# Optimization experiments

Measured on AMD Instinct MI355X. Metric: run time of the kernel, lower is better.

The kernel has to match this reference:

```python
import jax, jax.numpy as jnp
import numpy as np

B, S, DIM, H = 2, 2048, 2048, 16
HD = DIM // H  # head_dim = 128
EPS = 1e-6


def setup_inputs() -> dict:
    key = jax.random.key(0)
    ks = jax.random.split(key, 13)
    d = {
        'hidden_states': jax.random.normal(ks[0], (B, S, DIM), jnp.float32),
        'freqs_cos': jax.random.normal(ks[1], (1, S, 1, HD), jnp.float32),
        'freqs_sin': jax.random.normal(ks[2], (1, S, 1, HD), jnp.float32),
        'Wq': jax.random.normal(ks[3], (DIM, DIM), jnp.float32) * 0.02,
        'bq': jax.random.normal(ks[4], (DIM,), jnp.float32) * 0.02,
        'Wk': jax.random.normal(ks[5], (DIM, DIM), jnp.float32) * 0.02,
        'bk': jax.random.normal(ks[6], (DIM,), jnp.float32) * 0.02,
        'Wv': jax.random.normal(ks[7], (DIM, DIM), jnp.float32) * 0.02,
        'bv': jax.random.normal(ks[8], (DIM,), jnp.float32) * 0.02,
        'norm_q_w': jax.random.uniform(ks[9], (DIM,), jnp.float32, 0.5, 1.5),
        'norm_k_w': jax.random.uniform(ks[10], (DIM,), jnp.float32, 0.5, 1.5),
        'Wo': jax.random.normal(ks[11], (DIM, DIM), jnp.float32) * 0.02,
        'bo': jax.random.normal(ks[12], (DIM,), jnp.float32) * 0.02,
    }
    return d


def _rms_norm(x, w, eps=EPS):
    # local RMSNorm over the full inner_dim (no cross-rank reduce)
    xf = x.astype(jnp.float32)
    var = jnp.mean(xf * xf, axis=-1, keepdims=True)
    return (w * (xf * jax.lax.rsqrt(var + eps))).astype(x.dtype)


def _apply_rope(x, freqs_cos, freqs_sin):
    # x: [B,H,S,D]; freqs: [1,S,1,D] -> broadcast cos/sin at [1,1,S,D/2]
    dtype = x.dtype
    xf = x.astype(jnp.float32)
    x1 = xf[..., 0::2]
    x2 = xf[..., 1::2]
    cos = jnp.transpose(freqs_cos[..., 0::2], (0, 2, 1, 3)).astype(jnp.float32)
    sin = jnp.transpose(freqs_sin[..., 1::2], (0, 2, 1, 3)).astype(jnp.float32)
    even = x1 * cos - x2 * sin
    odd = x1 * sin + x2 * cos
    out = jnp.stack([even, odd], axis=-1).reshape(x.shape)
    return out.astype(dtype)


def reference(hidden_states, freqs_cos, freqs_sin, Wq, bq, Wk, bk, Wv, bv,
              norm_q_w, norm_k_w, Wo, bo):
    b, s, _ = hidden_states.shape
    q = hidden_states @ Wq.T + bq
    k = hidden_states @ Wk.T + bk
    v = hidden_states @ Wv.T + bv
    q = _rms_norm(q, norm_q_w)
    k = _rms_norm(k, norm_k_w)
    # [B,S,H*D] -> [B,H,S,D]
    q = q.reshape(b, s, H, HD).transpose(0, 2, 1, 3)
    k = k.reshape(b, s, H, HD).transpose(0, 2, 1, 3)
    v = v.reshape(b, s, H, HD).transpose(0, 2, 1, 3)
    q = _apply_rope(q, freqs_cos, freqs_sin)
    k = _apply_rope(k, freqs_cos, freqs_sin)
    # flash attention math (full, non-causal), scale = 1/sqrt(head_dim)
    scale = 1.0 / np.sqrt(HD).astype(np.float32)
    scores = jnp.einsum('bhqd,bhkd->bhqk', q, k) * scale
    attn = jax.nn.softmax(scores, axis=-1)
    out = jnp.einsum('bhqk,bhkd->bhqd', attn, v)
    out = out.transpose(0, 2, 1, 3).reshape(b, s, H * HD)
    return out @ Wo.T + bo
```

## Files before the change

### kernel.cpp

```cpp
#include <hip/hip_runtime.h>
#include <stdint.h>

#define DEVI __device__ __forceinline__

typedef __attribute__((ext_vector_type(8))) short bf16x8;
typedef __attribute__((ext_vector_type(4))) float f32x4;
typedef __attribute__((ext_vector_type(16))) float f32x16;
typedef __attribute__((ext_vector_type(4))) unsigned short u16x4;
typedef __attribute__((ext_vector_type(8))) unsigned short u16x8;

DEVI unsigned short f2bf(float f) {
    union { float f; unsigned u; } v; v.f = f;
    unsigned r = v.u + 0x7fffu + ((v.u >> 16) & 1u);
    return (unsigned short)(r >> 16);
}

DEVI float bf2f(unsigned short u) {
    union { unsigned u; float f; } v; v.u = ((unsigned)u) << 16;
    return v.f;
}

DEVI unsigned cvtpk(float lo, float hi) {
    unsigned r;
    asm("v_cvt_pk_bf16_f32 %0, %1, %2" : "=v"(r) : "v"(lo), "v"(hi));
    return r;
}

DEVI void gload16(const void* g, void* lds) {
    __builtin_amdgcn_global_load_lds(
        (const __attribute__((address_space(1))) unsigned int*)(uintptr_t)g,
        (__attribute__((address_space(3))) unsigned int*)(unsigned int)(uintptr_t)lds,
        16, 0, 0);
}

__global__ __launch_bounds__(256) void cvt_all(
    const float* __restrict__ hs, const float* __restrict__ wq,
    const float* __restrict__ wk, const float* __restrict__ wv,
    const float* __restrict__ wo,
    unsigned short* __restrict__ o_hs, unsigned short* __restrict__ o_wq,
    unsigned short* __restrict__ o_wk, unsigned short* __restrict__ o_wv,
    unsigned short* __restrict__ o_wo) {
    const int bid = blockIdx.x;
    const float* src; unsigned short* dst; int base;
    if (bid < 2048)      { src = hs; dst = o_hs; base = bid; }
    else if (bid < 3072) { src = wq; dst = o_wq; base = bid - 2048; }
    else if (bid < 4096) { src = wk; dst = o_wk; base = bid - 3072; }
    else if (bid < 5120) { src = wv; dst = o_wv; base = bid - 4096; }
    else                 { src = wo; dst = o_wo; base = bid - 5120; }
    const int i0 = base * 1024 + threadIdx.x;
#pragma unroll
    for (int k = 0; k < 4; k++) {
        const int i = i0 + k * 256;
        float4 v = ((const float4*)src)[i];
        u16x4 pk;
        pk[0] = f2bf(v.x); pk[1] = f2bf(v.y); pk[2] = f2bf(v.z); pk[3] = f2bf(v.w);
        ((u16x4*)dst)[i] = pk;
    }
}

DEVI void gemm_pipe_core(const unsigned short* __restrict__ A,
                         const unsigned short* __restrict__ Wt,
                         int m0, int n0, char* lds,
                         f32x4 (&acc)[2][2][2][2]) {
    constexpr int K = 2048;
    const int t = threadIdx.x;
    const int w = t >> 6, l = t & 63, lr = l & 15, lk = l >> 4;
    const int wr = w >> 2, wc = w & 3;
    const int sx = lr & 7;
    const int srow = t >> 3, sseg = (t & 7) ^ (srow & 7);
    const unsigned short* aS = A + (size_t)(m0 + srow) * K + sseg * 8;
    const unsigned short* bS = Wt + (size_t)(n0 + srow) * K + sseg * 8;
    char* Bbase = lds + 32768;

#pragma unroll
    for (int qm = 0; qm < 2; qm++)
#pragma unroll
        for (int qn = 0; qn < 2; qn++)
#pragma unroll
            for (int fr = 0; fr < 2; fr++)
#pragma unroll
                for (int fc = 0; fc < 2; fc++)
                    acc[qm][qn][fr][fc] = (f32x4){0.f, 0.f, 0.f, 0.f};

    auto STAGE = [&](int tt, int u) {
        if (tt >= 32) return;
        const int k0 = tt * 64, bb = tt & 1;
        if (u < 4)
            gload16(bS + (size_t)u * 64 * K + k0, Bbase + bb * 32768 + u * 8192 + w * 1024);
        else
            gload16(aS + (size_t)(u - 4) * 64 * K + k0, lds + bb * 16384 + (u - 4) * 8192 + w * 1024);
    };

    STAGE(0, 0); STAGE(0, 1); STAGE(0, 2); STAGE(0, 3); STAGE(0, 4); STAGE(0, 5);
    STAGE(1, 0); STAGE(1, 1); STAGE(1, 2);
    asm volatile("s_waitcnt vmcnt(3)" ::: "memory");
    __builtin_amdgcn_s_barrier();

    for (int kt = 0; kt < 32; ++kt) {
        const int bb = kt & 1;
        const char* Ab = lds + bb * 16384;
        const char* Bb = Bbase + bb * 32768;
        bf16x8 a0[2][2], a1[2][2], b0[2][2], b1[2][2];
#pragma unroll
        for (int fr = 0; fr < 2; fr++)
#pragma unroll
            for (int ks = 0; ks < 2; ks++) {
                a0[fr][ks] = *(const bf16x8*)(Ab + (wr * 64 + fr * 16 + lr) * 128 +
                                              (((ks * 4 + lk) ^ sx) << 4));
                a1[fr][ks] = *(const bf16x8*)(Ab + (wr * 64 + 32 + fr * 16 + lr) * 128 +
                                              (((ks * 4 + lk) ^ sx) << 4));
            }
#pragma unroll
        for (int fc = 0; fc < 2; fc++)
#pragma unroll
            for (int ks = 0; ks < 2; ks++) {
                b0[fc][ks] = *(const bf16x8*)(Bb + (wc * 64 + fc * 16 + lr) * 128 +
                                              (((ks * 4 + lk) ^ sx) << 4));
                b1[fc][ks] = *(const bf16x8*)(Bb + (wc * 64 + 32 + fc * 16 + lr) * 128 +
                                              (((ks * 4 + lk) ^ sx) << 4));
            }
        STAGE(kt + 1, 3); STAGE(kt + 1, 4); STAGE(kt + 1, 5);
        __builtin_amdgcn_s_setprio(1);
#pragma unroll
        for (int ks = 0; ks < 2; ks++)
#pragma unroll
            for (int fr = 0; fr < 2; fr++)
#pragma unroll
                for (int fc = 0; fc < 2; fc++) {
                    acc[0][0][fr][fc] = __builtin_amdgcn_mfma_f32_16x16x32_bf16(
                        a0[fr][ks], b0[fc][ks], acc[0][0][fr][fc], 0, 0, 0);
                    acc[1][0][fr][fc] = __builtin_amdgcn_mfma_f32_16x16x32_bf16(
                        a1[fr][ks], b0[fc][ks], acc[1][0][fr][fc], 0, 0, 0);
                }
        __builtin_amdgcn_s_setprio(0);
        asm volatile("s_waitcnt lgkmcnt(0)" ::: "memory");
        __builtin_amdgcn_s_barrier();
        STAGE(kt + 2, 0); STAGE(kt + 2, 1); STAGE(kt + 2, 2);
        __builtin_amdgcn_s_setprio(1);
#pragma unroll
        for (int ks = 0; ks < 2; ks++)
#pragma unroll
            for (int fr = 0; fr < 2; fr++)
#pragma unroll
                for (int fc = 0; fc < 2; fc++) {
                    acc[0][1][fr][fc] = __builtin_amdgcn_mfma_f32_16x16x32_bf16(
                        a0[fr][ks], b1[fc][ks], acc[0][1][fr][fc], 0, 0, 0);
                    acc[1][1][fr][fc] = __builtin_amdgcn_mfma_f32_16x16x32_bf16(
                        a1[fr][ks], b1[fc][ks], acc[1][1][fr][fc], 0, 0, 0);
                }
        __builtin_amdgcn_s_setprio(0);
        if (kt < 30)       asm volatile("s_waitcnt vmcnt(3)" ::: "memory");
        else if (kt == 30) asm volatile("s_waitcnt vmcnt(0)" ::: "memory");
        __builtin_amdgcn_s_barrier();
    }
}

__global__ __launch_bounds__(512, 2) void gemm_qkv(
    const unsigned short* __restrict__ A,
    const unsigned short* __restrict__ Wq16, const unsigned short* __restrict__ Wk16,
    const unsigned short* __restrict__ Wv16,
    const float* __restrict__ bq, const float* __restrict__ bk, const float* __restrict__ bv,
    unsigned short* __restrict__ qh, unsigned short* __restrict__ kh,
    unsigned short* __restrict__ Vt) {
    __shared__ char Lds[98304];
    const int bid = blockIdx.x;
    const int nt = bid & 7, rem = bid >> 3;
    const int mt = rem / 3, z = rem % 3;
    const int m0 = mt * 128, n0 = nt * 256;
    const unsigned short* W = (z == 0) ? Wq16 : (z == 1) ? Wk16 : Wv16;
    const float* bias = (z == 0) ? bq : (z == 1) ? bk : bv;

    f32x4 acc[2][2][2][2];
    gemm_pipe_core(A, W, m0, n0, Lds, acc);

    const int t = threadIdx.x, w = t >> 6, l = t & 63, lr = l & 15, lk = l >> 4;
    const int wr = w >> 2, wc = w & 3;
#pragma unroll
    for (int qm = 0; qm < 2; qm++)
#pragma unroll
        for (int qn = 0; qn < 2; qn++)
#pragma unroll
            for (int fr = 0; fr < 2; fr++)
#pragma unroll
                for (int fc = 0; fc < 2; fc++) {
                    const int col = n0 + wc * 64 + qn * 32 + fc * 16 + lr;
                    const int rb = m0 + wr * 64 + qm * 32 + fr * 16 + lk * 4;
                    const float bb = bias[col];
                    if (z == 2) {
                        const int hh = col >> 7, d = col & 127;
                        const int b = rb >> 11, s = rb & 2047;
                        u16x4 pk;
#pragma unroll
                        for (int j = 0; j < 4; j++) pk[j] = f2bf(acc[qm][qn][fr][fc][j] + bb);
                        *(u16x4*)(Vt + ((size_t)((b * 16 + hh) * 128 + d)) * 2048 + s) = pk;
                    } else {
                        unsigned short* out = (z == 0) ? qh : kh;
#pragma unroll
                        for (int j = 0; j < 4; j++)
                            out[(size_t)(rb + j) * 2048 + col] = f2bf(acc[qm][qn][fr][fc][j] + bb);
                    }
                }
}

__global__ __launch_bounds__(512, 2) void gemm_o(
    const unsigned short* __restrict__ A, const unsigned short* __restrict__ W16,
    const float* __restrict__ bo, float* __restrict__ out) {
    __shared__ char Lds[98304];
    const int bid = blockIdx.x;
    const int nt = bid & 7, mt = bid >> 3;
    const int m0 = mt * 128, n0 = nt * 256;

    f32x4 acc[2][2][2][2];
    gemm_pipe_core(A, W16, m0, n0, Lds, acc);

    const int t = threadIdx.x, w = t >> 6, l = t & 63, lr = l & 15, lk = l >> 4;
    const int wr = w >> 2, wc = w & 3;
#pragma unroll
    for (int qm = 0; qm < 2; qm++)
#pragma unroll
        for (int qn = 0; qn < 2; qn++)
#pragma unroll
            for (int fr = 0; fr < 2; fr++)
#pragma unroll
                for (int fc = 0; fc < 2; fc++) {
                    const int col = n0 + wc * 64 + qn * 32 + fc * 16 + lr;
                    const int rb = m0 + wr * 64 + qm * 32 + fr * 16 + lk * 4;
                    const float bb = bo[col];
#pragma unroll
                    for (int j = 0; j < 4; j++)
                        out[(size_t)(rb + j) * 2048 + col] = acc[qm][qn][fr][fc][j] + bb;
                }
}

__global__ __launch_bounds__(256) void norm_rope(
    const unsigned short* __restrict__ qh, const unsigned short* __restrict__ kh,
    const float* __restrict__ nqw, const float* __restrict__ nkw,
    const float* __restrict__ fc, const float* __restrict__ fs,
    unsigned short* __restrict__ Qr, unsigned short* __restrict__ Kr) {
    const int row = blockIdx.x;
    const int which = blockIdx.y;
    const unsigned short* in = which ? kh : qh;
    const float* wv = which ? nkw : nqw;
    unsigned short* out = which ? Kr : Qr;
    const float qs = which ? 1.0f : 0.12751744f;
    const int t = threadIdx.x;
    u16x8 xr = *(const u16x8*)(in + (size_t)row * 2048 + t * 8);
    float xv[8];
#pragma unroll
    for (int e = 0; e < 8; e++) xv[e] = bf2f(xr[e]);
    float ss = 0.f;
#pragma unroll
    for (int e = 0; e < 8; e++) ss += xv[e] * xv[e];
#pragma unroll
    for (int m = 1; m < 64; m <<= 1) ss += __shfl_xor(ss, m, 64);
    __shared__ float red[4];
    if ((t & 63) == 0) red[t >> 6] = ss;
    __syncthreads();
    const float tot = red[0] + red[1] + red[2] + red[3];
    const float r = rsqrtf(tot * (1.0f / 2048.0f) + 1e-6f);
    const int s = row & 2047, b = row >> 11;
    const int d0 = t * 8, hd0 = d0 & 127, h = d0 >> 7;
    float4 c0 = ((const float4*)(fc + s * 128 + hd0))[0];
    float4 c1 = ((const float4*)(fc + s * 128 + hd0))[1];
    float4 s0 = ((const float4*)(fs + s * 128 + hd0))[0];
    float4 s1 = ((const float4*)(fs + s * 128 + hd0))[1];
    float4 w0 = ((const float4*)(wv + d0))[0];
    float4 w1 = ((const float4*)(wv + d0))[1];
    float wn[8] = {w0.x, w0.y, w0.z, w0.w, w1.x, w1.y, w1.z, w1.w};
    float xn[8];
#pragma unroll
    for (int e = 0; e < 8; e++) xn[e] = xv[e] * wn[e] * r;
    float o[8];
    o[0] = xn[0] * c0.x - xn[1] * s0.y;  o[1] = xn[0] * s0.y + xn[1] * c0.x;
    o[2] = xn[2] * c0.z - xn[3] * s0.w;  o[3] = xn[2] * s0.w + xn[3] * c0.z;
    o[4] = xn[4] * c1.x - xn[5] * s1.y;  o[5] = xn[4] * s1.y + xn[5] * c1.x;
    o[6] = xn[6] * c1.z - xn[7] * s1.w;  o[7] = xn[6] * s1.w + xn[7] * c1.z;
    u16x8 pk;
#pragma unroll
    for (int e = 0; e < 8; e++) pk[e] = f2bf(o[e] * qs);
    *(u16x8*)(out + ((size_t)((b * 16 + h) * 2048 + s)) * 128 + hd0) = pk;
}

__global__ __launch_bounds__(256, 2) void attn(
    const unsigned short* __restrict__ Qr, const unsigned short* __restrict__ Kr,
    const unsigned short* __restrict__ Vt, unsigned short* __restrict__ Ao) {
    __shared__ unsigned short Kl[2][64 * 128];
    __shared__ unsigned short Vl[2][128 * 64];
    const int t = threadIdx.x, w = t >> 6, l = t & 63;
    const int ql = l & 31, h = l >> 5;
    const int bid = blockIdx.x;
    const int xcd = bid & 7, idx = bid >> 3;
    const int bh = xcd * 4 + (idx >> 4);
    const int q0 = (idx & 15) * 128 + w * 32;
    const int b = bh >> 4, head = bh & 15;

    const unsigned short* Qp = Qr + ((size_t)bh * 2048 + q0) * 128;
    bf16x8 qf[8];
#pragma unroll
    for (int c8 = 0; c8 < 8; c8++)
        qf[c8] = *(const bf16x8*)(Qp + ql * 128 + c8 * 16 + h * 8);

    f32x16 accO[4];
#pragma unroll
    for (int dt = 0; dt < 4; dt++)
#pragma unroll
        for (int r = 0; r < 16; r++) accO[dt][r] = 0.f;
    float mj = -1e30f, ljp = 0.f;

    const unsigned short* Kb = Kr + (size_t)bh * 2048 * 128;
    const unsigned short* Vb = Vt + (size_t)bh * 128 * 2048;
    const int krow = t >> 4, kseg = (t & 15) ^ (krow & 7);
    const int vrow = t >> 3, vseg = (t & 7) ^ (vrow & 7);

    auto STAGE = [&](int buf, int kv0) {
        char* kd = (char*)&Kl[buf][0] + w * 1024;
        char* vd = (char*)&Vl[buf][0] + w * 1024;
#pragma unroll
        for (int c = 0; c < 4; c++)
            gload16(Kb + (size_t)(kv0 + c * 16 + krow) * 128 + kseg * 8, kd + c * 4096);
#pragma unroll
        for (int c = 0; c < 4; c++)
            gload16(Vb + (size_t)(c * 32 + vrow) * 2048 + kv0 + vseg * 8, vd + c * 4096);
    };

    const int qx = ql & 7;
    STAGE(0, 0);
    __syncthreads();
    int cur = 0;
    for (int it = 0; it < 32; ++it) {
        if (it < 31) STAGE(cur ^ 1, (it + 1) * 64);
        f32x16 S0, S1;
#pragma unroll
        for (int r = 0; r < 16; r++) { S0[r] = 0.f; S1[r] = 0.f; }
        __builtin_amdgcn_s_setprio(1);
#pragma unroll
        for (int c8 = 0; c8 < 8; c8++) {
            const int sg = ((c8 * 2 + h) ^ qx) << 4;
            bf16x8 k0 = *(const bf16x8*)((const char*)&Kl[cur][0] + ql * 256 + sg);
            bf16x8 k1 = *(const bf16x8*)((const char*)&Kl[cur][0] + (32 + ql) * 256 + sg);
            S0 = __builtin_amdgcn_mfma_f32_32x32x16_bf16(k0, qf[c8], S0, 0, 0, 0);
            S1 = __builtin_amdgcn_mfma_f32_32x32x16_bf16(k1, qf[c8], S1, 0, 0, 0);
        }
        __builtin_amdgcn_s_setprio(0);
        float mloc = S0[0];
#pragma unroll
        for (int r = 1; r < 16; r++) mloc = fmaxf(mloc, S0[r]);
#pragma unroll
        for (int r = 0; r < 16; r++) mloc = fmaxf(mloc, S1[r]);
        const float mx = fmaxf(mloc, __shfl_xor(mloc, 32, 64));
        if (!__all(mx <= mj + 8.0f)) {
            const float mn = fmaxf(mj, mx);
            const float corr = exp2f(mj - mn);
            mj = mn;
            ljp *= corr;
#pragma unroll
            for (int dt = 0; dt < 4; dt++)
#pragma unroll
                for (int r = 0; r < 16; r++) accO[dt][r] *= corr;
        }
        unsigned W[16];
        float lsum = 0.f;
#pragma unroll
        for (int i = 0; i < 8; i++) {
            const float pa = exp2f(S0[2 * i] - mj);
            const float pb = exp2f(S0[2 * i + 1] - mj);
            W[i] = cvtpk(pa, pb);
            lsum += pa + pb;
        }
#pragma unroll
        for (int i = 0; i < 8; i++) {
            const float pa = exp2f(S1[2 * i] - mj);
            const float pb = exp2f(S1[2 * i + 1] - mj);
            W[8 + i] = cvtpk(pa, pb);
            lsum += pa + pb;
        }
        ljp += lsum;
#pragma unroll
        for (int c = 0; c < 2; c++) {
            unsigned X[8];
#pragma unroll
            for (int i = 0; i < 8; i++)
                X[i] = (unsigned)__shfl_xor((int)W[c * 8 + i], 32, 64);
            union U { unsigned u[4]; bf16x8 v; };
            U F, G;
            F.u[0] = h ? X[2] : W[c * 8 + 0];
            F.u[1] = h ? X[3] : W[c * 8 + 1];
            F.u[2] = h ? W[c * 8 + 2] : X[0];
            F.u[3] = h ? W[c * 8 + 3] : X[1];
            G.u[0] = h ? X[6] : W[c * 8 + 4];
            G.u[1] = h ? X[7] : W[c * 8 + 5];
            G.u[2] = h ? W[c * 8 + 6] : X[4];
            G.u[3] = h ? W[c * 8 + 7] : X[5];
            __builtin_amdgcn_s_setprio(1);
#pragma unroll
            for (int dt = 0; dt < 4; dt++) {
                const int sg = (((2 * c) * 2 + h) ^ qx) << 4;
                bf16x8 vf = *(const bf16x8*)((const char*)&Vl[cur][0] + (dt * 32 + ql) * 128 + sg);
                accO[dt] = __builtin_amdgcn_mfma_f32_32x32x16_bf16(vf, F.v, accO[dt], 0, 0, 0);
            }
#pragma unroll
            for (int dt = 0; dt < 4; dt++) {
                const int sg = (((2 * c + 1) * 2 + h) ^ qx) << 4;
                bf16x8 vf = *(const bf16x8*)((const char*)&Vl[cur][0] + (dt * 32 + ql) * 128 + sg);
                accO[dt] = __builtin_amdgcn_mfma_f32_32x32x16_bf16(vf, G.v, accO[dt], 0, 0, 0);
            }
            __builtin_amdgcn_s_setprio(0);
        }
        __syncthreads();
        cur ^= 1;
    }
    const float lj = ljp + __shfl_xor(ljp, 32, 64);
    const float inv = 1.0f / lj;
    unsigned short* ob = Ao + ((size_t)(b * 2048 + q0 + ql)) * 2048 + head * 128;
#pragma unroll
    for (int dt = 0; dt < 4; dt++)
#pragma unroll
        for (int i = 0; i < 8; i++) {
            const float a = accO[dt][2 * i] * inv;
            const float c = accO[dt][2 * i + 1] * inv;
            const int d = dt * 32 + ((2 * i) & 3) + 8 * (i >> 1) + 4 * h;
            *(unsigned*)(ob + d) = cvtpk(a, c);
        }
}

extern "C" void kernel_launch(void* const* d_in, const int* in_sizes, int n_in,
                              void* d_out, int out_size, void* d_ws, size_t ws_size,
                              hipStream_t stream) {
    const float* hs  = (const float*)d_in[0];
    const float* fc  = (const float*)d_in[1];
    const float* fs  = (const float*)d_in[2];
    const float* Wq  = (const float*)d_in[3];
    const float* bq  = (const float*)d_in[4];
    const float* Wk  = (const float*)d_in[5];
    const float* bk  = (const float*)d_in[6];
    const float* Wv  = (const float*)d_in[7];
    const float* bv  = (const float*)d_in[8];
    const float* nqw = (const float*)d_in[9];
    const float* nkw = (const float*)d_in[10];
    const float* Wo  = (const float*)d_in[11];
    const float* bo  = (const float*)d_in[12];
    float* out = (float*)d_out;

    char* p = (char*)d_ws;
    unsigned short* hs16 = (unsigned short*)p; p += (size_t)8388608 * 2;
    unsigned short* Wq16 = (unsigned short*)p; p += (size_t)4194304 * 2;
    unsigned short* Wk16 = (unsigned short*)p; p += (size_t)4194304 * 2;
    unsigned short* Wv16 = (unsigned short*)p; p += (size_t)4194304 * 2;
    unsigned short* Wo16 = (unsigned short*)p; p += (size_t)4194304 * 2;
    unsigned short* qh = (unsigned short*)p;   p += (size_t)8388608 * 2;
    unsigned short* kh = (unsigned short*)p;   p += (size_t)8388608 * 2;
    unsigned short* Qr = (unsigned short*)p;   p += (size_t)8388608 * 2;
    unsigned short* Kr = (unsigned short*)p;   p += (size_t)8388608 * 2;
    unsigned short* Vt = (unsigned short*)p;   p += (size_t)8388608 * 2;
    unsigned short* Ao = (unsigned short*)p;   p += (size_t)8388608 * 2;
    (void)ws_size; (void)in_sizes; (void)n_in; (void)out_size;

    cvt_all<<<6144, 256, 0, stream>>>(hs, Wq, Wk, Wv, Wo,
                                      hs16, Wq16, Wk16, Wv16, Wo16);
    gemm_qkv<<<768, 512, 0, stream>>>(hs16, Wq16, Wk16, Wv16,
                                      bq, bk, bv, qh, kh, Vt);
    norm_rope<<<dim3(4096, 2), 256, 0, stream>>>(qh, kh, nqw, nkw, fc, fs, Qr, Kr);
    attn<<<512, 256, 0, stream>>>(Qr, Kr, Vt, Ao);
    gemm_o<<<256, 512, 0, stream>>>(Ao, Wo16, bo, out);
}
```

Before: 297.5 us.

## Use 256x256 output tiles with a new pipelined core for QKV GEMM

Adds a new GEMM core that computes 256x256 output tiles per block, each wave holding an 8x4 grid of 16x16 MFMA accumulators, with double-buffered LDS of 128KB. The QKV projection grid is halved to 384 blocks and the block index mapping changes so the M tile comes first. The aim is higher arithmetic intensity per LDS and global load, which cuts A/B reloads. In exchange it uses more registers and LDS per block, so occupancy drops, and 384 blocks may fill the 256 CUs unevenly.

```diff
diff --git a/kernel.cpp b/kernel.cpp
--- a/kernel.cpp
+++ b/kernel.cpp
@@ -58,6 +58,83 @@
     }
 }
 
+DEVI void gemm_core256(const unsigned short* __restrict__ A,
+                       const unsigned short* __restrict__ Wt,
+                       int m0, int n0, char* lds,
+                       f32x4 (&acc)[8][4]) {
+    constexpr int K = 2048;
+    const int t = threadIdx.x;
+    const int w = t >> 6, l = t & 63, lr = l & 15, lk = l >> 4;
+    const int wr = w >> 2, wc = w & 3;
+    const int sx = lr & 7;
+    const int srow = t >> 3, sseg = (t & 7) ^ (srow & 7);
+    const unsigned short* aS = A + (size_t)(m0 + srow) * K + sseg * 8;
+    const unsigned short* bS = Wt + (size_t)(n0 + srow) * K + sseg * 8;
+
+#pragma unroll
+    for (int mi = 0; mi < 8; mi++)
+#pragma unroll
+        for (int ni = 0; ni < 4; ni++) acc[mi][ni] = (f32x4){0.f, 0.f, 0.f, 0.f};
+
+    auto STAGE = [&](int tt, int u) {
+        if (tt >= 32) return;
+        const int k0 = tt * 64, bb = tt & 1;
+        if (u < 4)
+            gload16(aS + (size_t)u * 64 * K + k0, lds + bb * 32768 + u * 8192 + w * 1024);
+        else
+            gload16(bS + (size_t)(u - 4) * 64 * K + k0,
+                    lds + 65536 + bb * 32768 + (u - 4) * 8192 + w * 1024);
+    };
+
+    STAGE(0, 0); STAGE(0, 1); STAGE(0, 2); STAGE(0, 3);
+    STAGE(0, 4); STAGE(0, 5); STAGE(0, 6); STAGE(0, 7);
+    STAGE(1, 0); STAGE(1, 1); STAGE(1, 2); STAGE(1, 3);
+    asm volatile("s_waitcnt vmcnt(4)" ::: "memory");
+    __builtin_amdgcn_s_barrier();
+
+    for (int kt = 0; kt < 32; ++kt) {
+        const int bb = kt & 1;
+        const char* Ab = lds + bb * 32768;
+        const char* Bb = lds + 65536 + bb * 32768;
+        bf16x8 a[8][2], b[4][2];
+#pragma unroll
+        for (int mi = 0; mi < 8; mi++)
+#pragma unroll
+            for (int ks = 0; ks < 2; ks++)
+                a[mi][ks] = *(const bf16x8*)(Ab + (wr * 128 + mi * 16 + lr) * 128 +
+                                             (((ks * 4 + lk) ^ sx) << 4));
+#pragma unroll
+        for (int ni = 0; ni < 4; ni++)
+#pragma unroll
+            for (int ks = 0; ks < 2; ks++)
+                b[ni][ks] = *(const bf16x8*)(Bb + (wc * 64 + ni * 16 + lr) * 128 +
+                                             (((ks * 4 + lk) ^ sx) << 4));
+        STAGE(kt + 1, 4); STAGE(kt + 1, 5); STAGE(kt + 1, 6); STAGE(kt + 1, 7);
+        __builtin_amdgcn_s_setprio(1);
+#pragma unroll
+        for (int mi = 0; mi < 8; mi++)
+#pragma unroll
+            for (int ni = 0; ni < 4; ni++)
+                acc[mi][ni] = __builtin_amdgcn_mfma_f32_16x16x32_bf16(
+                    a[mi][0], b[ni][0], acc[mi][ni], 0, 0, 0);
+        __builtin_amdgcn_s_setprio(0);
+        asm volatile("s_waitcnt lgkmcnt(0)" ::: "memory");
+        __builtin_amdgcn_s_barrier();
+        STAGE(kt + 2, 0); STAGE(kt + 2, 1); STAGE(kt + 2, 2); STAGE(kt + 2, 3);
+        __builtin_amdgcn_s_setprio(1);
+#pragma unroll
+        for (int mi = 0; mi < 8; mi++)
+#pragma unroll
+            for (int ni = 0; ni < 4; ni++)
+                acc[mi][ni] = __builtin_amdgcn_mfma_f32_16x16x32_bf16(
+                    a[mi][1], b[ni][1], acc[mi][ni], 0, 0, 0);
+        __builtin_amdgcn_s_setprio(0);
+        if (kt < 30)       asm volatile("s_waitcnt vmcnt(4)" ::: "memory");
+        else if (kt == 30) asm volatile("s_waitcnt vmcnt(0)" ::: "memory");
+        __builtin_amdgcn_s_barrier();
+    }
+}
+
 DEVI void gemm_pipe_core(const unsigned short* __restrict__ A,
                          const unsigned short* __restrict__ Wt,
                          int m0, int n0, char* lds,
@@ -162,44 +239,40 @@
     const float* __restrict__ bq, const float* __restrict__ bk, const float* __restrict__ bv,
     unsigned short* __restrict__ qh, unsigned short* __restrict__ kh,
     unsigned short* __restrict__ Vt) {
-    __shared__ char Lds[98304];
+    __shared__ char Lds[131072];
     const int bid = blockIdx.x;
-    const int nt = bid & 7, rem = bid >> 3;
-    const int mt = rem / 3, z = rem % 3;
-    const int m0 = mt * 128, n0 = nt * 256;
+    const int nt = bid & 7, idx = bid >> 3;
+    const int mt = idx & 15, z = idx >> 4;
+    const int m0 = mt * 256, n0 = nt * 256;
     const unsigned short* W = (z == 0) ? Wq16 : (z == 1) ? Wk16 : Wv16;
     const float* bias = (z == 0) ? bq : (z == 1) ? bk : bv;
 
-    f32x4 acc[2][2][2][2];
-    gemm_pipe_core(A, W, m0, n0, Lds, acc);
+    f32x4 acc[8][4];
+    gemm_core256(A, W, m0, n0, Lds, acc);
 
     const int t = threadIdx.x, w = t >> 6, l = t & 63, lr = l & 15, lk = l >> 4;
     const int wr = w >> 2, wc = w & 3;
 #pragma unroll
-    for (int qm = 0; qm < 2; qm++)
-#pragma unroll
-        for (int qn = 0; qn < 2; qn++)
-#pragma unroll
-            for (int fr = 0; fr < 2; fr++)
-#pragma unroll
-                for (int fc = 0; fc < 2; fc++) {
-                    const int col = n0 + wc * 64 + qn * 32 + fc * 16 + lr;
-                    const int rb = m0 + wr * 64 + qm * 32 + fr * 16 + lk * 4;
-                    const float bb = bias[col];
-                    if (z == 2) {
-                        const int hh = col >> 7, d = col & 127;
-                        const int b = rb >> 11, s = rb & 2047;
-                        u16x4 pk;
-#pragma unroll
-                        for (int j = 0; j < 4; j++) pk[j] = f2bf(acc[qm][qn][fr][fc][j] + bb);
-                        *(u16x4*)(Vt + ((size_t)((b * 16 + hh) * 128 + d)) * 2048 + s) = pk;
-                    } else {
-                        unsigned short* out = (z == 0) ? qh : kh;
-#pragma unroll
-                        for (int j = 0; j < 4; j++)
-                            out[(size_t)(rb + j) * 2048 + col] = f2bf(acc[qm][qn][fr][fc][j] + bb);
-                    }
-                }
+    for (int mi = 0; mi < 8; mi++)
+#pragma unroll
+        for (int ni = 0; ni < 4; ni++) {
+            const int col = n0 + wc * 64 + ni * 16 + lr;
+            const int rb = m0 + wr * 128 + mi * 16 + lk * 4;
+            const float bb = bias[col];
+            if (z == 2) {
+                const int hh = col >> 7, d = col & 127;
+                const int b = rb >> 11, s = rb & 2047;
+                u16x4 pk;
+#pragma unroll
+                for (int j = 0; j < 4; j++) pk[j] = f2bf(acc[mi][ni][j] + bb);
+                *(u16x4*)(Vt + ((size_t)((b * 16 + hh) * 128 + d)) * 2048 + s) = pk;
+            } else {
+                unsigned short* out = (z == 0) ? qh : kh;
+#pragma unroll
+                for (int j = 0; j < 4; j++)
+                    out[(size_t)(rb + j) * 2048 + col] = f2bf(acc[mi][ni][j] + bb);
+            }
+        }
 }
 
 __global__ __launch_bounds__(512, 2) void gemm_o(
@@ -457,7 +530,7 @@
 
     cvt_all<<<6144, 256, 0, stream>>>(hs, Wq, Wk, Wv, Wo,
                                       hs16, Wq16, Wk16, Wv16, Wo16);
-    gemm_qkv<<<768, 512, 0, stream>>>(hs16, Wq16, Wk16, Wv16,
+    gemm_qkv<<<384, 512, 0, stream>>>(hs16, Wq16, Wk16, Wv16,
                                       bq, bk, bv, qh, kh, Vt);
     norm_rope<<<dim3(4096, 2), 256, 0, stream>>>(qh, kh, nqw, nkw, fc, fs, Qr, Kr);
     attn<<<512, 256, 0, stream>>>(Qr, Kr, Vt, Ao);
```

Result: no change. 298.5 us (+0.3%).
